# Kernel tuning notes

Measured on AMD Instinct MI355X. Metric: run time of the kernel, lower is better.

## Reference

```python
import jax, jax.numpy as jnp
import numpy as np
import math

B, H, L, D = 2, 16, 2048, 128


def setup_inputs() -> dict:
    key = jax.random.key(0)
    kq, kk, kv, km, kp = jax.random.split(key, 5)
    q = jax.random.normal(kq, (B, H, L, D), dtype=jnp.float32)
    k = jax.random.normal(kk, (B, H, L, D), dtype=jnp.float32)
    v = jax.random.normal(kv, (B, H, L, D), dtype=jnp.float32)
    mask = jax.random.randint(km, (B, 1, L, L), 0, 2, dtype=jnp.int32)
    probs = jax.random.uniform(kp, (B, L, L), dtype=jnp.float32)
    alpha = jnp.ones((), dtype=jnp.float32)  # learned scalar Parameter, init 1.0
    return {"q": q, "k": k, "v": v, "mask": mask, "probs": probs, "alpha": alpha}


def reference(q, k, v, mask, probs, alpha):
    # scores: (B, H, L, L)
    scale = 1.0 / math.sqrt(q.shape[-1])
    attn_score = jnp.einsum("bhqd,bhkd->bhqk", q, k) * scale
    # additive learned-scale probability bias, broadcast over heads
    attn_score = attn_score + probs[:, None, :, :] * alpha
    # masked_fill(mask == 0, -inf)
    attn_score = jnp.where(mask == 0, -jnp.inf, attn_score)
    attn_p = jax.nn.softmax(attn_score, axis=-1)
    # dropout p=0.0 -> identity
    attention = jnp.einsum("bhqk,bhkd->bhqd", attn_p, v)
    return attention, attn_p
```

## Files before the change

### kernel.cpp

```cpp
#include <hip/hip_runtime.h>

constexpr int BB = 2, HH = 16, LL = 2048, DD = 128;
constexpr int QB = 64, KB = 32, NKT = LL / KB;
constexpr float SCALE = 0.08838834764831845f;

typedef __attribute__((ext_vector_type(8))) short bf16x8;
typedef __attribute__((ext_vector_type(8))) unsigned short u16x8;
typedef __attribute__((ext_vector_type(4))) float f32x4;
typedef __attribute__((ext_vector_type(4))) int i32x4;

static __device__ __forceinline__ unsigned short f2bf(float f) {
  unsigned int u = __builtin_bit_cast(unsigned int, f);
  u += 0x7fffu + ((u >> 16) & 1u);
  return (unsigned short)(u >> 16);
}
static __device__ __forceinline__ float bf2f(unsigned short h) {
  return __builtin_bit_cast(float, (unsigned int)h << 16);
}

#define GLD16(gsrc, ldst) __builtin_amdgcn_global_load_lds( \
    (const __attribute__((address_space(1))) void*)(gsrc), \
    (__attribute__((address_space(3))) void*)(ldst), 16, 0, 0)

__global__ __launch_bounds__(256)
void prep_kernel(const float* __restrict__ k, const float* __restrict__ v,
                 const int* __restrict__ mask, const float* __restrict__ probs,
                 const float* __restrict__ alphap,
                 unsigned short* __restrict__ kbT, unsigned short* __restrict__ vtT,
                 unsigned short* __restrict__ biasW)
{
  __shared__ unsigned short sT[128 * 40];
  const int bid = blockIdx.x;
  const int bh = bid >> 6, kt = bid & 63;
  const int t = threadIdx.x;
  const float alpha = alphap[0];
  const size_t tileBase = (size_t)bid * 4096;
  const float* kg = k + ((size_t)bh * LL + kt * 32) * DD;
  const float* vg = v + ((size_t)bh * LL + kt * 32) * DD;

  #pragma unroll
  for (int s = t; s < 512; s += 256) {
    int dsl = s >> 5, key = s & 31;
    const float* src = kg + key * DD + dsl * 8;
    float4 a = *(const float4*)src;
    float4 c = *(const float4*)(src + 4);
    u16x8 w;
    w[0] = f2bf(a.x); w[1] = f2bf(a.y); w[2] = f2bf(a.z); w[3] = f2bf(a.w);
    w[4] = f2bf(c.x); w[5] = f2bf(c.y); w[6] = f2bf(c.z); w[7] = f2bf(c.w);
    *(u16x8*)(kbT + tileBase + (size_t)s * 8) = w;
  }
  #pragma unroll
  for (int i = 0; i < 4; ++i) {
    int idx = i * 256 + t;
    int key = idx >> 5, d4 = (idx & 31) * 4;
    float4 x = ((const float4*)vg)[idx];
    sT[(d4 + 0) * 40 + key] = f2bf(x.x);
    sT[(d4 + 1) * 40 + key] = f2bf(x.y);
    sT[(d4 + 2) * 40 + key] = f2bf(x.z);
    sT[(d4 + 3) * 40 + key] = f2bf(x.w);
  }
  #pragma unroll
  for (int it = 0; it < 2; ++it) {
    int tileIdx = bid * 2 + it;
    int b = tileIdx >> 11;
    int rem = tileIdx & 2047;
    int tq = rem >> 6;
    int tk = rem & 63;
    int row = ((t >> 6) << 4) + (t & 15);
    int kc = ((t >> 4) & 3) * 4;
    const float* pr = probs + (size_t)b * LL * LL + (size_t)(tq * 64 + row) * LL + tk * 32;
    const int* mr = mask + (size_t)b * LL * LL + (size_t)(tq * 64 + row) * LL + tk * 32;
    float4 f0 = *(const float4*)(pr + kc);
    float4 f1 = *(const float4*)(pr + kc + 16);
    int4 m0 = *(const int4*)(mr + kc);
    int4 m1 = *(const int4*)(mr + kc + 16);
    u16x8 o;
    o[0] = f2bf(m0.x ? f0.x * alpha : -1e30f);
    o[1] = f2bf(m0.y ? f0.y * alpha : -1e30f);
    o[2] = f2bf(m0.z ? f0.z * alpha : -1e30f);
    o[3] = f2bf(m0.w ? f0.w * alpha : -1e30f);
    o[4] = f2bf(m1.x ? f1.x * alpha : -1e30f);
    o[5] = f2bf(m1.y ? f1.y * alpha : -1e30f);
    o[6] = f2bf(m1.z ? f1.z * alpha : -1e30f);
    o[7] = f2bf(m1.w ? f1.w * alpha : -1e30f);
    *(u16x8*)(biasW + (size_t)tileIdx * 2048 + t * 8) = o;
  }
  __syncthreads();
  #pragma unroll
  for (int s = t; s < 512; s += 256) {
    int kc = s >> 7, d = s & 127;
    u16x8 w = *(const u16x8*)&sT[d * 40 + kc * 8];
    *(u16x8*)(vtT + tileBase + (size_t)s * 8) = w;
  }
}

__global__ __launch_bounds__(256, 6)
void passA_kernel(const float* __restrict__ q, const unsigned short* __restrict__ kbT,
                  const unsigned short* __restrict__ biasW, float* __restrict__ invW)
{
  __shared__ unsigned short sK[2][4096];

  const int tid = threadIdx.x;
  const int lane = tid & 63;
  const int wid = tid >> 6;
  const int l15 = lane & 15;
  const int l4 = lane >> 4;

  const int bid = blockIdx.x;
  const int work = ((bid & 7) << 7) | (bid >> 3);
  const int bh = work >> 5;
  const int qt = work & 31;
  const int b = bh >> 4;
  const int q0 = qt * QB;
  const int row16 = wid << 4;

  const unsigned short* kbh = kbT + (size_t)bh * 64 * 4096;
  const unsigned short* bg = biasW + ((size_t)(b * 32 + qt) * 64) * 2048 + (wid << 9) + (lane << 3);

  bf16x8 qf0, qf1, qf2, qf3;
  {
    const float* qs = q + (size_t)(bh * LL + q0 + row16 + l15) * DD + l4 * 8;
    #define LQ(FR, KC) { \
      float4 a = *(const float4*)(qs + (KC) * 32); \
      float4 c = *(const float4*)(qs + (KC) * 32 + 4); \
      FR[0]=(short)f2bf(a.x); FR[1]=(short)f2bf(a.y); FR[2]=(short)f2bf(a.z); FR[3]=(short)f2bf(a.w); \
      FR[4]=(short)f2bf(c.x); FR[5]=(short)f2bf(c.y); FR[6]=(short)f2bf(c.z); FR[7]=(short)f2bf(c.w); }
    LQ(qf0, 0) LQ(qf1, 1) LQ(qf2, 2) LQ(qf3, 3)
    #undef LQ
  }

  #define DMA_K(BUF, KT) do { \
    GLD16(kbh + (size_t)(KT) * 4096 + tid * 8,         &sK[BUF][wid << 9]); \
    GLD16(kbh + (size_t)(KT) * 4096 + (256 + tid) * 8, &sK[BUF][2048 + (wid << 9)]); } while (0)

  #define QKS(KC, QF) { \
    bf16x8 k0 = *(const bf16x8*)&sK[cur][(((KC) * 4 + l4) * 32 + l15) * 8]; \
    a0 = __builtin_amdgcn_mfma_f32_16x16x32_bf16(k0, QF, a0, 0, 0, 0); \
    bf16x8 k1 = *(const bf16x8*)&sK[cur][(((KC) * 4 + l4) * 32 + 16 + l15) * 8]; \
    a1 = __builtin_amdgcn_mfma_f32_16x16x32_bf16(k1, QF, a1, 0, 0, 0); }

  DMA_K(0, 0);
  u16x8 cnb = *(const u16x8*)(bg);
  float sum = 0.f;
  for (int kt = 0; kt < NKT; ++kt) {
    const int cur = kt & 1;
    __syncthreads();
    if (kt + 1 < NKT) DMA_K(cur ^ 1, kt + 1);
    u16x8 bt = cnb;
    if (kt + 1 < NKT) cnb = *(const u16x8*)(bg + (size_t)(kt + 1) * 2048);
    f32x4 a0 = {0.f,0.f,0.f,0.f}, a1 = {0.f,0.f,0.f,0.f};
    QKS(0, qf0) QKS(1, qf1) QKS(2, qf2) QKS(3, qf3)
    sum += __expf(a0[0] * SCALE + bf2f(bt[0]));
    sum += __expf(a0[1] * SCALE + bf2f(bt[1]));
    sum += __expf(a0[2] * SCALE + bf2f(bt[2]));
    sum += __expf(a0[3] * SCALE + bf2f(bt[3]));
    sum += __expf(a1[0] * SCALE + bf2f(bt[4]));
    sum += __expf(a1[1] * SCALE + bf2f(bt[5]));
    sum += __expf(a1[2] * SCALE + bf2f(bt[6]));
    sum += __expf(a1[3] * SCALE + bf2f(bt[7]));
  }
  sum += __shfl_xor(sum, 16, 64);
  sum += __shfl_xor(sum, 32, 64);
  if (l4 == 0)
    invW[(size_t)bh * LL + q0 + row16 + l15] = 1.0f / sum;
  #undef DMA_K
  #undef QKS
}

__global__ __launch_bounds__(256, 4)
void passB_kernel(const float* __restrict__ q, const unsigned short* __restrict__ kbT,
                  const unsigned short* __restrict__ vtT, const unsigned short* __restrict__ biasW,
                  const float* __restrict__ invW,
                  float* __restrict__ outA, float* __restrict__ outP)
{
  __shared__ unsigned short sK[2][4096];
  __shared__ unsigned short sVt[2][4096];

  const int tid = threadIdx.x;
  const int lane = tid & 63;
  const int wid = tid >> 6;
  const int l15 = lane & 15;
  const int l4 = lane >> 4;

  const int bid = blockIdx.x;
  const int work = ((bid & 7) << 7) | (bid >> 3);
  const int bh = work >> 5;
  const int qt = work & 31;
  const int b = bh >> 4;
  const int q0 = qt * QB;
  const int row16 = wid << 4;

  const unsigned short* kbh = kbT + (size_t)bh * 64 * 4096;
  const unsigned short* vbh = vtT + (size_t)bh * 64 * 4096;
  const unsigned short* bg = biasW + ((size_t)(b * 32 + qt) * 64) * 2048 + (wid << 9) + (lane << 3);
  float* oA = outA + (size_t)(bh * LL + q0) * DD;
  float* oPr = outP + (size_t)bh * LL * LL + (size_t)(q0 + row16 + l15) * LL;

  const float inv = invW[(size_t)bh * LL + q0 + row16 + l15];

  bf16x8 qf0, qf1, qf2, qf3;
  {
    const float* qs = q + (size_t)(bh * LL + q0 + row16 + l15) * DD + l4 * 8;
    #define LQ(FR, KC) { \
      float4 a = *(const float4*)(qs + (KC) * 32); \
      float4 c = *(const float4*)(qs + (KC) * 32 + 4); \
      FR[0]=(short)f2bf(a.x); FR[1]=(short)f2bf(a.y); FR[2]=(short)f2bf(a.z); FR[3]=(short)f2bf(a.w); \
      FR[4]=(short)f2bf(c.x); FR[5]=(short)f2bf(c.y); FR[6]=(short)f2bf(c.z); FR[7]=(short)f2bf(c.w); }
    LQ(qf0, 0) LQ(qf1, 1) LQ(qf2, 2) LQ(qf3, 3)
    #undef LQ
  }

  #define DMA_K(BUF, KT) do { \
    GLD16(kbh + (size_t)(KT) * 4096 + tid * 8,         &sK[BUF][wid << 9]); \
    GLD16(kbh + (size_t)(KT) * 4096 + (256 + tid) * 8, &sK[BUF][2048 + (wid << 9)]); } while (0)
  #define DMA_V(BUF, KT) do { \
    GLD16(vbh + (size_t)(KT) * 4096 + tid * 8,         &sVt[BUF][wid << 9]); \
    GLD16(vbh + (size_t)(KT) * 4096 + (256 + tid) * 8, &sVt[BUF][2048 + (wid << 9)]); } while (0)

  #define QKS(KC, QF) { \
    bf16x8 k0 = *(const bf16x8*)&sK[cur][(((KC) * 4 + l4) * 32 + l15) * 8]; \
    a0 = __builtin_amdgcn_mfma_f32_16x16x32_bf16(k0, QF, a0, 0, 0, 0); \
    bf16x8 k1 = *(const bf16x8*)&sK[cur][(((KC) * 4 + l4) * 32 + 16 + l15) * 8]; \
    a1 = __builtin_amdgcn_mfma_f32_16x16x32_bf16(k1, QF, a1, 0, 0, 0); }

  const int srcA = l15 + (((l4 << 1) + 0) & 3) * 16;
  const int srcB = l15 + (((l4 << 1) + 1) & 3) * 16;
  const bool hiTile = (l4 >= 2);

  f32x4 oacc[8];
  #pragma unroll
  for (int dt = 0; dt < 8; ++dt) oacc[dt] = (f32x4){0.f,0.f,0.f,0.f};

  u16x8 cnb;

  #define BBODY(KT) do { \
    const int cur = (KT) & 1; \
    u16x8 bt = cnb; \
    if ((KT) + 1 < NKT) cnb = *(const u16x8*)(bg + (size_t)((KT) + 1) * 2048); \
    f32x4 a0 = {0.f,0.f,0.f,0.f}, a1 = {0.f,0.f,0.f,0.f}; \
    QKS(0, qf0) QKS(1, qf1) QKS(2, qf2) QKS(3, qf3) \
    f32x4 p0, p1; \
    p0[0] = __expf(a0[0] * SCALE + bf2f(bt[0])) * inv; \
    p0[1] = __expf(a0[1] * SCALE + bf2f(bt[1])) * inv; \
    p0[2] = __expf(a0[2] * SCALE + bf2f(bt[2])) * inv; \
    p0[3] = __expf(a0[3] * SCALE + bf2f(bt[3])) * inv; \
    p1[0] = __expf(a1[0] * SCALE + bf2f(bt[4])) * inv; \
    p1[1] = __expf(a1[1] * SCALE + bf2f(bt[5])) * inv; \
    p1[2] = __expf(a1[2] * SCALE + bf2f(bt[6])) * inv; \
    p1[3] = __expf(a1[3] * SCALE + bf2f(bt[7])) * inv; \
    __builtin_nontemporal_store(p0, (f32x4*)(oPr + (KT) * 32 + (l4 << 2))); \
    __builtin_nontemporal_store(p1, (f32x4*)(oPr + (KT) * 32 + 16 + (l4 << 2))); \
    unsigned d00, d01, d10, d11; \
    asm("v_cvt_pk_bf16_f32 %0, %1, %2" : "=v"(d00) : "v"(p0[0]), "v"(p0[1])); \
    asm("v_cvt_pk_bf16_f32 %0, %1, %2" : "=v"(d01) : "v"(p0[2]), "v"(p0[3])); \
    asm("v_cvt_pk_bf16_f32 %0, %1, %2" : "=v"(d10) : "v"(p1[0]), "v"(p1[1])); \
    asm("v_cvt_pk_bf16_f32 %0, %1, %2" : "=v"(d11) : "v"(p1[2]), "v"(p1[3])); \
    int a00 = __shfl((int)d00, srcA, 64); \
    int a01 = __shfl((int)d01, srcA, 64); \
    int a02 = __shfl((int)d00, srcB, 64); \
    int a03 = __shfl((int)d01, srcB, 64); \
    int b00 = __shfl((int)d10, srcA, 64); \
    int b01 = __shfl((int)d11, srcA, 64); \
    int b02 = __shfl((int)d10, srcB, 64); \
    int b03 = __shfl((int)d11, srcB, 64); \
    i32x4 fw; \
    fw[0] = hiTile ? b00 : a00; \
    fw[1] = hiTile ? b01 : a01; \
    fw[2] = hiTile ? b02 : a02; \
    fw[3] = hiTile ? b03 : a03; \
    bf16x8 aP = __builtin_bit_cast(bf16x8, fw); \
    _Pragma("unroll") \
    for (int dt = 0; dt < 8; ++dt) { \
      bf16x8 bV = *(const bf16x8*)&sVt[cur][(l4 * 128 + dt * 16 + l15) * 8]; \
      oacc[dt] = __builtin_amdgcn_mfma_f32_16x16x32_bf16(aP, bV, oacc[dt], 0, 0, 0); \
    } \
  } while (0)

  cnb = *(const u16x8*)(bg);
  DMA_K(0, 0); DMA_V(0, 0);
  asm volatile("s_waitcnt vmcnt(0)\n\ts_barrier" ::: "memory");
  DMA_K(1, 1); DMA_V(1, 1);
  BBODY(0);
  for (int kt = 1; kt < NKT; ++kt) {
    asm volatile("s_waitcnt vmcnt(2)\n\ts_barrier" ::: "memory");
    if (kt + 1 < NKT) {
      const int c2 = (kt + 1) & 1;
      DMA_K(c2, kt + 1); DMA_V(c2, kt + 1);
    }
    BBODY(kt);
  }

  #pragma unroll
  for (int dt = 0; dt < 8; ++dt) {
    #pragma unroll
    for (int r = 0; r < 4; ++r) {
      __builtin_nontemporal_store(oacc[dt][r],
          oA + (size_t)(row16 + (l4 << 2) + r) * DD + dt * 16 + l15);
    }
  }
}

extern "C" void kernel_launch(void* const* d_in, const int* in_sizes, int n_in,
                              void* d_out, int out_size, void* d_ws, size_t ws_size,
                              hipStream_t stream) {
  const float* q = (const float*)d_in[0];
  const float* k = (const float*)d_in[1];
  const float* v = (const float*)d_in[2];
  const int* mask = (const int*)d_in[3];
  const float* probs = (const float*)d_in[4];
  const float* alpha = (const float*)d_in[5];
  float* outA = (float*)d_out;
  float* outP = outA + (size_t)BB * HH * LL * DD;
  unsigned short* kbT = (unsigned short*)d_ws;
  unsigned short* vtT = kbT + (size_t)32 * 64 * 4096;
  unsigned short* biasW = vtT + (size_t)32 * 64 * 4096;
  float* invW = (float*)(biasW + (size_t)4096 * 2048);
  hipLaunchKernelGGL(prep_kernel, dim3(32 * 64), dim3(256), 0, stream,
                     k, v, mask, probs, alpha, kbT, vtT, biasW);
  hipLaunchKernelGGL(passA_kernel, dim3(BB * HH * (LL / QB)), dim3(256), 0, stream,
                     q, kbT, biasW, invW);
  hipLaunchKernelGGL(passB_kernel, dim3(BB * HH * (LL / QB)), dim3(256), 0, stream,
                     q, kbT, vtT, biasW, invW, outA, outP);
}
```

Before: 257.8 us.

## Switch attention passes to 32x32x16 MFMA with two-wave blocks

Replaces the 16x16x32 bf16 MFMA tiles in both softmax passes with 32x32x16 MFMA, so each wave now owns 32 query rows and blocks shrink to 128 threads. The bias workspace layout in the prep kernel is permuted to match the new accumulator layout, and the P-to-A-operand reshuffle becomes a single xor-32 swap. The aim is to cut LDS K/V fragment reads and shuffle overhead per flop. In exchange each thread holds more accumulator registers, and the probability stores become narrower strided writes.

```diff
diff --git a/kernel.cpp b/kernel.cpp
--- a/kernel.cpp
+++ b/kernel.cpp
@@ -7,6 +7,7 @@
 typedef __attribute__((ext_vector_type(8))) short bf16x8;
 typedef __attribute__((ext_vector_type(8))) unsigned short u16x8;
 typedef __attribute__((ext_vector_type(4))) float f32x4;
+typedef __attribute__((ext_vector_type(16))) float f32x16;
 typedef __attribute__((ext_vector_type(4))) int i32x4;
 
 static __device__ __forceinline__ unsigned short f2bf(float f) {
@@ -61,19 +62,22 @@
   }
   #pragma unroll
   for (int it = 0; it < 2; ++it) {
-    int tileIdx = bid * 2 + it;
-    int b = tileIdx >> 11;
-    int rem = tileIdx & 2047;
-    int tq = rem >> 6;
-    int tk = rem & 63;
-    int row = ((t >> 6) << 4) + (t & 15);
-    int kc = ((t >> 4) & 3) * 4;
-    const float* pr = probs + (size_t)b * LL * LL + (size_t)(tq * 64 + row) * LL + tk * 32;
-    const int* mr = mask + (size_t)b * LL * LL + (size_t)(tq * 64 + row) * LL + tk * 32;
-    float4 f0 = *(const float4*)(pr + kc);
-    float4 f1 = *(const float4*)(pr + kc + 16);
-    int4 m0 = *(const int4*)(mr + kc);
-    int4 m1 = *(const int4*)(mr + kc + 16);
+    int ti = bid * 2 + it;
+    int b = ti >> 11;
+    int tq = (ti >> 6) & 31;
+    int tk = ti & 63;
+    int wv = t >> 7;
+    int ln = (t >> 1) & 63;
+    int rh = t & 1;
+    int l31 = ln & 31, hi = ln >> 5;
+    int qrow = tq * 64 + wv * 32 + l31;
+    int kbase = tk * 32 + 4 * hi + rh * 16;
+    const float* pr = probs + (size_t)b * LL * LL + (size_t)qrow * LL + kbase;
+    const int* mr = mask + (size_t)b * LL * LL + (size_t)qrow * LL + kbase;
+    float4 f0 = *(const float4*)(pr);
+    float4 f1 = *(const float4*)(pr + 8);
+    int4 m0 = *(const int4*)(mr);
+    int4 m1 = *(const int4*)(mr + 8);
     u16x8 o;
     o[0] = f2bf(m0.x ? f0.x * alpha : -1e30f);
     o[1] = f2bf(m0.y ? f0.y * alpha : -1e30f);
@@ -83,7 +87,7 @@
     o[5] = f2bf(m1.y ? f1.y * alpha : -1e30f);
     o[6] = f2bf(m1.z ? f1.z * alpha : -1e30f);
     o[7] = f2bf(m1.w ? f1.w * alpha : -1e30f);
-    *(u16x8*)(biasW + (size_t)tileIdx * 2048 + t * 8) = o;
+    *(u16x8*)(biasW + (size_t)ti * 2048 + wv * 1024 + ln * 16 + rh * 8) = o;
   }
   __syncthreads();
   #pragma unroll
@@ -94,80 +98,104 @@
   }
 }
 
-__global__ __launch_bounds__(256, 6)
+#define ZERO16 {0.f,0.f,0.f,0.f,0.f,0.f,0.f,0.f,0.f,0.f,0.f,0.f,0.f,0.f,0.f,0.f}
+
+#define COMMON_DECODE \
+  const int tid = threadIdx.x; \
+  const int lane = tid & 63; \
+  const int wid = tid >> 6; \
+  const int l31 = lane & 31; \
+  const int hi5 = lane >> 5; \
+  const int bid = blockIdx.x; \
+  const int work = ((bid & 7) << 7) | (bid >> 3); \
+  const int bh = work >> 5; \
+  const int qt = work & 31; \
+  const int b = bh >> 4; \
+  const int q0 = qt * QB; \
+  const int qrow = q0 + wid * 32 + l31;
+
+#define LOAD_QFRAGS \
+  bf16x8 qf0, qf1, qf2, qf3, qf4, qf5, qf6, qf7; \
+  { \
+    const float* qs = q + (size_t)(bh * LL + qrow) * DD + hi5 * 8; \
+    _Pragma("unroll") \
+    for (int m = 0; m < 8; ++m) { \
+      float4 a = *(const float4*)(qs + m * 16); \
+      float4 c = *(const float4*)(qs + m * 16 + 4); \
+      u16x8 w; \
+      w[0]=f2bf(a.x); w[1]=f2bf(a.y); w[2]=f2bf(a.z); w[3]=f2bf(a.w); \
+      w[4]=f2bf(c.x); w[5]=f2bf(c.y); w[6]=f2bf(c.z); w[7]=f2bf(c.w); \
+      bf16x8 f = __builtin_bit_cast(bf16x8, w); \
+      switch (m) { case 0: qf0=f; break; case 1: qf1=f; break; \
+                   case 2: qf2=f; break; case 3: qf3=f; break; \
+                   case 4: qf4=f; break; case 5: qf5=f; break; \
+                   case 6: qf6=f; break; default: qf7=f; } \
+    } \
+  }
+
+#define DMA_T(ARR, BASE, KT) do { \
+  _Pragma("unroll") \
+  for (int i_ = 0; i_ < 4; ++i_) \
+    GLD16((BASE) + (size_t)(KT) * 4096 + (i_ * 128 + tid) * 8, \
+          &ARR[i_ * 1024 + (tid >> 6) * 512]); } while (0)
+
+#define QK32(SBUF) \
+  f32x16 s = ZERO16; \
+  { \
+    bf16x8 kf; \
+    kf = *(const bf16x8*)&SBUF[(( 0 + hi5) * 32 + l31) * 8]; \
+    s = __builtin_amdgcn_mfma_f32_32x32x16_bf16(kf, qf0, s, 0, 0, 0); \
+    kf = *(const bf16x8*)&SBUF[(( 2 + hi5) * 32 + l31) * 8]; \
+    s = __builtin_amdgcn_mfma_f32_32x32x16_bf16(kf, qf1, s, 0, 0, 0); \
+    kf = *(const bf16x8*)&SBUF[(( 4 + hi5) * 32 + l31) * 8]; \
+    s = __builtin_amdgcn_mfma_f32_32x32x16_bf16(kf, qf2, s, 0, 0, 0); \
+    kf = *(const bf16x8*)&SBUF[(( 6 + hi5) * 32 + l31) * 8]; \
+    s = __builtin_amdgcn_mfma_f32_32x32x16_bf16(kf, qf3, s, 0, 0, 0); \
+    kf = *(const bf16x8*)&SBUF[(( 8 + hi5) * 32 + l31) * 8]; \
+    s = __builtin_amdgcn_mfma_f32_32x32x16_bf16(kf, qf4, s, 0, 0, 0); \
+    kf = *(const bf16x8*)&SBUF[((10 + hi5) * 32 + l31) * 8]; \
+    s = __builtin_amdgcn_mfma_f32_32x32x16_bf16(kf, qf5, s, 0, 0, 0); \
+    kf = *(const bf16x8*)&SBUF[((12 + hi5) * 32 + l31) * 8]; \
+    s = __builtin_amdgcn_mfma_f32_32x32x16_bf16(kf, qf6, s, 0, 0, 0); \
+    kf = *(const bf16x8*)&SBUF[((14 + hi5) * 32 + l31) * 8]; \
+    s = __builtin_amdgcn_mfma_f32_32x32x16_bf16(kf, qf7, s, 0, 0, 0); \
+  }
+
+__global__ __launch_bounds__(128, 4)
 void passA_kernel(const float* __restrict__ q, const unsigned short* __restrict__ kbT,
                   const unsigned short* __restrict__ biasW, float* __restrict__ invW)
 {
   __shared__ unsigned short sK[2][4096];
-
-  const int tid = threadIdx.x;
-  const int lane = tid & 63;
-  const int wid = tid >> 6;
-  const int l15 = lane & 15;
-  const int l4 = lane >> 4;
-
-  const int bid = blockIdx.x;
-  const int work = ((bid & 7) << 7) | (bid >> 3);
-  const int bh = work >> 5;
-  const int qt = work & 31;
-  const int b = bh >> 4;
-  const int q0 = qt * QB;
-  const int row16 = wid << 4;
-
+  COMMON_DECODE
   const unsigned short* kbh = kbT + (size_t)bh * 64 * 4096;
-  const unsigned short* bg = biasW + ((size_t)(b * 32 + qt) * 64) * 2048 + (wid << 9) + (lane << 3);
-
-  bf16x8 qf0, qf1, qf2, qf3;
-  {
-    const float* qs = q + (size_t)(bh * LL + q0 + row16 + l15) * DD + l4 * 8;
-    #define LQ(FR, KC) { \
-      float4 a = *(const float4*)(qs + (KC) * 32); \
-      float4 c = *(const float4*)(qs + (KC) * 32 + 4); \
-      FR[0]=(short)f2bf(a.x); FR[1]=(short)f2bf(a.y); FR[2]=(short)f2bf(a.z); FR[3]=(short)f2bf(a.w); \
-      FR[4]=(short)f2bf(c.x); FR[5]=(short)f2bf(c.y); FR[6]=(short)f2bf(c.z); FR[7]=(short)f2bf(c.w); }
-    LQ(qf0, 0) LQ(qf1, 1) LQ(qf2, 2) LQ(qf3, 3)
-    #undef LQ
-  }
-
-  #define DMA_K(BUF, KT) do { \
-    GLD16(kbh + (size_t)(KT) * 4096 + tid * 8,         &sK[BUF][wid << 9]); \
-    GLD16(kbh + (size_t)(KT) * 4096 + (256 + tid) * 8, &sK[BUF][2048 + (wid << 9)]); } while (0)
-
-  #define QKS(KC, QF) { \
-    bf16x8 k0 = *(const bf16x8*)&sK[cur][(((KC) * 4 + l4) * 32 + l15) * 8]; \
-    a0 = __builtin_amdgcn_mfma_f32_16x16x32_bf16(k0, QF, a0, 0, 0, 0); \
-    bf16x8 k1 = *(const bf16x8*)&sK[cur][(((KC) * 4 + l4) * 32 + 16 + l15) * 8]; \
-    a1 = __builtin_amdgcn_mfma_f32_16x16x32_bf16(k1, QF, a1, 0, 0, 0); }
-
-  DMA_K(0, 0);
-  u16x8 cnb = *(const u16x8*)(bg);
+  const unsigned short* bg = biasW + ((size_t)(b * 32 + qt) * 64) * 2048 + wid * 1024 + lane * 16;
+  LOAD_QFRAGS
+
+  DMA_T(sK[0], kbh, 0);
+  u16x8 cb0 = *(const u16x8*)(bg);
+  u16x8 cb1 = *(const u16x8*)(bg + 8);
   float sum = 0.f;
   for (int kt = 0; kt < NKT; ++kt) {
     const int cur = kt & 1;
     __syncthreads();
-    if (kt + 1 < NKT) DMA_K(cur ^ 1, kt + 1);
-    u16x8 bt = cnb;
-    if (kt + 1 < NKT) cnb = *(const u16x8*)(bg + (size_t)(kt + 1) * 2048);
-    f32x4 a0 = {0.f,0.f,0.f,0.f}, a1 = {0.f,0.f,0.f,0.f};
-    QKS(0, qf0) QKS(1, qf1) QKS(2, qf2) QKS(3, qf3)
-    sum += __expf(a0[0] * SCALE + bf2f(bt[0]));
-    sum += __expf(a0[1] * SCALE + bf2f(bt[1]));
-    sum += __expf(a0[2] * SCALE + bf2f(bt[2]));
-    sum += __expf(a0[3] * SCALE + bf2f(bt[3]));
-    sum += __expf(a1[0] * SCALE + bf2f(bt[4]));
-    sum += __expf(a1[1] * SCALE + bf2f(bt[5]));
-    sum += __expf(a1[2] * SCALE + bf2f(bt[6]));
-    sum += __expf(a1[3] * SCALE + bf2f(bt[7]));
-  }
-  sum += __shfl_xor(sum, 16, 64);
+    if (kt + 1 < NKT) DMA_T(sK[cur ^ 1], kbh, kt + 1);
+    u16x8 b0 = cb0, b1 = cb1;
+    if (kt + 1 < NKT) {
+      cb0 = *(const u16x8*)(bg + (size_t)(kt + 1) * 2048);
+      cb1 = *(const u16x8*)(bg + (size_t)(kt + 1) * 2048 + 8);
+    }
+    QK32(sK[cur])
+    #pragma unroll
+    for (int r = 0; r < 8; ++r) sum += __expf(s[r] * SCALE + bf2f(b0[r]));
+    #pragma unroll
+    for (int r = 0; r < 8; ++r) sum += __expf(s[r + 8] * SCALE + bf2f(b1[r]));
+  }
   sum += __shfl_xor(sum, 32, 64);
-  if (l4 == 0)
-    invW[(size_t)bh * LL + q0 + row16 + l15] = 1.0f / sum;
-  #undef DMA_K
-  #undef QKS
-}
-
-__global__ __launch_bounds__(256, 4)
+  if (lane < 32)
+    invW[(size_t)bh * LL + qrow] = 1.0f / sum;
+}
+
+__global__ __launch_bounds__(128, 3)
 void passB_kernel(const float* __restrict__ q, const unsigned short* __restrict__ kbT,
                   const unsigned short* __restrict__ vtT, const unsigned short* __restrict__ biasW,
                   const float* __restrict__ invW,
@@ -175,129 +203,109 @@
 {
   __shared__ unsigned short sK[2][4096];
   __shared__ unsigned short sVt[2][4096];
-
-  const int tid = threadIdx.x;
-  const int lane = tid & 63;
-  const int wid = tid >> 6;
-  const int l15 = lane & 15;
-  const int l4 = lane >> 4;
-
-  const int bid = blockIdx.x;
-  const int work = ((bid & 7) << 7) | (bid >> 3);
-  const int bh = work >> 5;
-  const int qt = work & 31;
-  const int b = bh >> 4;
-  const int q0 = qt * QB;
-  const int row16 = wid << 4;
-
+  COMMON_DECODE
   const unsigned short* kbh = kbT + (size_t)bh * 64 * 4096;
   const unsigned short* vbh = vtT + (size_t)bh * 64 * 4096;
-  const unsigned short* bg = biasW + ((size_t)(b * 32 + qt) * 64) * 2048 + (wid << 9) + (lane << 3);
+  const unsigned short* bg = biasW + ((size_t)(b * 32 + qt) * 64) * 2048 + wid * 1024 + lane * 16;
   float* oA = outA + (size_t)(bh * LL + q0) * DD;
-  float* oPr = outP + (size_t)bh * LL * LL + (size_t)(q0 + row16 + l15) * LL;
-
-  const float inv = invW[(size_t)bh * LL + q0 + row16 + l15];
-
-  bf16x8 qf0, qf1, qf2, qf3;
-  {
-    const float* qs = q + (size_t)(bh * LL + q0 + row16 + l15) * DD + l4 * 8;
-    #define LQ(FR, KC) { \
-      float4 a = *(const float4*)(qs + (KC) * 32); \
-      float4 c = *(const float4*)(qs + (KC) * 32 + 4); \
-      FR[0]=(short)f2bf(a.x); FR[1]=(short)f2bf(a.y); FR[2]=(short)f2bf(a.z); FR[3]=(short)f2bf(a.w); \
-      FR[4]=(short)f2bf(c.x); FR[5]=(short)f2bf(c.y); FR[6]=(short)f2bf(c.z); FR[7]=(short)f2bf(c.w); }
-    LQ(qf0, 0) LQ(qf1, 1) LQ(qf2, 2) LQ(qf3, 3)
-    #undef LQ
-  }
-
-  #define DMA_K(BUF, KT) do { \
-    GLD16(kbh + (size_t)(KT) * 4096 + tid * 8,         &sK[BUF][wid << 9]); \
-    GLD16(kbh + (size_t)(KT) * 4096 + (256 + tid) * 8, &sK[BUF][2048 + (wid << 9)]); } while (0)
-  #define DMA_V(BUF, KT) do { \
-    GLD16(vbh + (size_t)(KT) * 4096 + tid * 8,         &sVt[BUF][wid << 9]); \
-    GLD16(vbh + (size_t)(KT) * 4096 + (256 + tid) * 8, &sVt[BUF][2048 + (wid << 9)]); } while (0)
-
-  #define QKS(KC, QF) { \
-    bf16x8 k0 = *(const bf16x8*)&sK[cur][(((KC) * 4 + l4) * 32 + l15) * 8]; \
-    a0 = __builtin_amdgcn_mfma_f32_16x16x32_bf16(k0, QF, a0, 0, 0, 0); \
-    bf16x8 k1 = *(const bf16x8*)&sK[cur][(((KC) * 4 + l4) * 32 + 16 + l15) * 8]; \
-    a1 = __builtin_amdgcn_mfma_f32_16x16x32_bf16(k1, QF, a1, 0, 0, 0); }
-
-  const int srcA = l15 + (((l4 << 1) + 0) & 3) * 16;
-  const int srcB = l15 + (((l4 << 1) + 1) & 3) * 16;
-  const bool hiTile = (l4 >= 2);
-
-  f32x4 oacc[8];
-  #pragma unroll
-  for (int dt = 0; dt < 8; ++dt) oacc[dt] = (f32x4){0.f,0.f,0.f,0.f};
-
-  u16x8 cnb;
+  float* oPr = outP + (size_t)bh * LL * LL + (size_t)qrow * LL;
+  const float inv = invW[(size_t)bh * LL + qrow];
+  LOAD_QFRAGS
+
+  f32x16 acc0 = ZERO16, acc1 = ZERO16, acc2 = ZERO16, acc3 = ZERO16;
+  u16x8 cb0, cb1;
 
   #define BBODY(KT) do { \
     const int cur = (KT) & 1; \
-    u16x8 bt = cnb; \
-    if ((KT) + 1 < NKT) cnb = *(const u16x8*)(bg + (size_t)((KT) + 1) * 2048); \
-    f32x4 a0 = {0.f,0.f,0.f,0.f}, a1 = {0.f,0.f,0.f,0.f}; \
-    QKS(0, qf0) QKS(1, qf1) QKS(2, qf2) QKS(3, qf3) \
-    f32x4 p0, p1; \
-    p0[0] = __expf(a0[0] * SCALE + bf2f(bt[0])) * inv; \
-    p0[1] = __expf(a0[1] * SCALE + bf2f(bt[1])) * inv; \
-    p0[2] = __expf(a0[2] * SCALE + bf2f(bt[2])) * inv; \
-    p0[3] = __expf(a0[3] * SCALE + bf2f(bt[3])) * inv; \
-    p1[0] = __expf(a1[0] * SCALE + bf2f(bt[4])) * inv; \
-    p1[1] = __expf(a1[1] * SCALE + bf2f(bt[5])) * inv; \
-    p1[2] = __expf(a1[2] * SCALE + bf2f(bt[6])) * inv; \
-    p1[3] = __expf(a1[3] * SCALE + bf2f(bt[7])) * inv; \
-    __builtin_nontemporal_store(p0, (f32x4*)(oPr + (KT) * 32 + (l4 << 2))); \
-    __builtin_nontemporal_store(p1, (f32x4*)(oPr + (KT) * 32 + 16 + (l4 << 2))); \
-    unsigned d00, d01, d10, d11; \
-    asm("v_cvt_pk_bf16_f32 %0, %1, %2" : "=v"(d00) : "v"(p0[0]), "v"(p0[1])); \
-    asm("v_cvt_pk_bf16_f32 %0, %1, %2" : "=v"(d01) : "v"(p0[2]), "v"(p0[3])); \
-    asm("v_cvt_pk_bf16_f32 %0, %1, %2" : "=v"(d10) : "v"(p1[0]), "v"(p1[1])); \
-    asm("v_cvt_pk_bf16_f32 %0, %1, %2" : "=v"(d11) : "v"(p1[2]), "v"(p1[3])); \
-    int a00 = __shfl((int)d00, srcA, 64); \
-    int a01 = __shfl((int)d01, srcA, 64); \
-    int a02 = __shfl((int)d00, srcB, 64); \
-    int a03 = __shfl((int)d01, srcB, 64); \
-    int b00 = __shfl((int)d10, srcA, 64); \
-    int b01 = __shfl((int)d11, srcA, 64); \
-    int b02 = __shfl((int)d10, srcB, 64); \
-    int b03 = __shfl((int)d11, srcB, 64); \
-    i32x4 fw; \
-    fw[0] = hiTile ? b00 : a00; \
-    fw[1] = hiTile ? b01 : a01; \
-    fw[2] = hiTile ? b02 : a02; \
-    fw[3] = hiTile ? b03 : a03; \
-    bf16x8 aP = __builtin_bit_cast(bf16x8, fw); \
+    u16x8 b0 = cb0, b1 = cb1; \
+    if ((KT) + 1 < NKT) { \
+      cb0 = *(const u16x8*)(bg + (size_t)((KT) + 1) * 2048); \
+      cb1 = *(const u16x8*)(bg + (size_t)((KT) + 1) * 2048 + 8); \
+    } \
+    QK32(sK[cur]) \
+    f32x16 p; \
     _Pragma("unroll") \
-    for (int dt = 0; dt < 8; ++dt) { \
-      bf16x8 bV = *(const bf16x8*)&sVt[cur][(l4 * 128 + dt * 16 + l15) * 8]; \
-      oacc[dt] = __builtin_amdgcn_mfma_f32_16x16x32_bf16(aP, bV, oacc[dt], 0, 0, 0); \
+    for (int r = 0; r < 8; ++r) p[r] = __expf(s[r] * SCALE + bf2f(b0[r])) * inv; \
+    _Pragma("unroll") \
+    for (int r = 0; r < 8; ++r) p[r + 8] = __expf(s[r + 8] * SCALE + bf2f(b1[r])) * inv; \
+     \
+    { \
+      f32x4 st; \
+      st[0]=p[0];  st[1]=p[1];  st[2]=p[2];  st[3]=p[3]; \
+      __builtin_nontemporal_store(st, (f32x4*)(oPr + (KT) * 32 + 4 * hi5)); \
+      st[0]=p[4];  st[1]=p[5];  st[2]=p[6];  st[3]=p[7]; \
+      __builtin_nontemporal_store(st, (f32x4*)(oPr + (KT) * 32 + 8 + 4 * hi5)); \
+      st[0]=p[8];  st[1]=p[9];  st[2]=p[10]; st[3]=p[11]; \
+      __builtin_nontemporal_store(st, (f32x4*)(oPr + (KT) * 32 + 16 + 4 * hi5)); \
+      st[0]=p[12]; st[1]=p[13]; st[2]=p[14]; st[3]=p[15]; \
+      __builtin_nontemporal_store(st, (f32x4*)(oPr + (KT) * 32 + 24 + 4 * hi5)); \
     } \
+     \
+    unsigned D0,D1,D2,D3,D4,D5,D6,D7; \
+    asm("v_cvt_pk_bf16_f32 %0, %1, %2" : "=v"(D0) : "v"(p[0]),  "v"(p[1])); \
+    asm("v_cvt_pk_bf16_f32 %0, %1, %2" : "=v"(D1) : "v"(p[2]),  "v"(p[3])); \
+    asm("v_cvt_pk_bf16_f32 %0, %1, %2" : "=v"(D2) : "v"(p[4]),  "v"(p[5])); \
+    asm("v_cvt_pk_bf16_f32 %0, %1, %2" : "=v"(D3) : "v"(p[6]),  "v"(p[7])); \
+    asm("v_cvt_pk_bf16_f32 %0, %1, %2" : "=v"(D4) : "v"(p[8]),  "v"(p[9])); \
+    asm("v_cvt_pk_bf16_f32 %0, %1, %2" : "=v"(D5) : "v"(p[10]), "v"(p[11])); \
+    asm("v_cvt_pk_bf16_f32 %0, %1, %2" : "=v"(D6) : "v"(p[12]), "v"(p[13])); \
+    asm("v_cvt_pk_bf16_f32 %0, %1, %2" : "=v"(D7) : "v"(p[14]), "v"(p[15])); \
+    int X0 = __shfl_xor((int)D0, 32, 64), X1 = __shfl_xor((int)D1, 32, 64); \
+    int X2 = __shfl_xor((int)D2, 32, 64), X3 = __shfl_xor((int)D3, 32, 64); \
+    int X4 = __shfl_xor((int)D4, 32, 64), X5 = __shfl_xor((int)D5, 32, 64); \
+    int X6 = __shfl_xor((int)D6, 32, 64), X7 = __shfl_xor((int)D7, 32, 64); \
+    const bool lo = (hi5 == 0); \
+    i32x4 w0, w1; \
+    w0[0] = lo ? (int)D0 : X2;  w0[1] = lo ? (int)D1 : X3; \
+    w0[2] = lo ? X0 : (int)D2;  w0[3] = lo ? X1 : (int)D3; \
+    w1[0] = lo ? (int)D4 : X6;  w1[1] = lo ? (int)D5 : X7; \
+    w1[2] = lo ? X4 : (int)D6;  w1[3] = lo ? X5 : (int)D7; \
+    bf16x8 aP0 = __builtin_bit_cast(bf16x8, w0); \
+    bf16x8 aP1 = __builtin_bit_cast(bf16x8, w1); \
+     \
+    bf16x8 bV; \
+    bV = *(const bf16x8*)&sVt[cur][((0 + hi5) * 128 +  0 + l31) * 8]; \
+    acc0 = __builtin_amdgcn_mfma_f32_32x32x16_bf16(aP0, bV, acc0, 0, 0, 0); \
+    bV = *(const bf16x8*)&sVt[cur][((2 + hi5) * 128 +  0 + l31) * 8]; \
+    acc0 = __builtin_amdgcn_mfma_f32_32x32x16_bf16(aP1, bV, acc0, 0, 0, 0); \
+    bV = *(const bf16x8*)&sVt[cur][((0 + hi5) * 128 + 32 + l31) * 8]; \
+    acc1 = __builtin_amdgcn_mfma_f32_32x32x16_bf16(aP0, bV, acc1, 0, 0, 0); \
+    bV = *(const bf16x8*)&sVt[cur][((2 + hi5) * 128 + 32 + l31) * 8]; \
+    acc1 = __builtin_amdgcn_mfma_f32_32x32x16_bf16(aP1, bV, acc1, 0, 0, 0); \
+    bV = *(const bf16x8*)&sVt[cur][((0 + hi5) * 128 + 64 + l31) * 8]; \
+    acc2 = __builtin_amdgcn_mfma_f32_32x32x16_bf16(aP0, bV, acc2, 0, 0, 0); \
+    bV = *(const bf16x8*)&sVt[cur][((2 + hi5) * 128 + 64 + l31) * 8]; \
+    acc2 = __builtin_amdgcn_mfma_f32_32x32x16_bf16(aP1, bV, acc2, 0, 0, 0); \
+    bV = *(const bf16x8*)&sVt[cur][((0 + hi5) * 128 + 96 + l31) * 8]; \
+    acc3 = __builtin_amdgcn_mfma_f32_32x32x16_bf16(aP0, bV, acc3, 0, 0, 0); \
+    bV = *(const bf16x8*)&sVt[cur][((2 + hi5) * 128 + 96 + l31) * 8]; \
+    acc3 = __builtin_amdgcn_mfma_f32_32x32x16_bf16(aP1, bV, acc3, 0, 0, 0); \
   } while (0)
 
-  cnb = *(const u16x8*)(bg);
-  DMA_K(0, 0); DMA_V(0, 0);
+  cb0 = *(const u16x8*)(bg);
+  cb1 = *(const u16x8*)(bg + 8);
+  DMA_T(sK[0], kbh, 0); DMA_T(sVt[0], vbh, 0);
   asm volatile("s_waitcnt vmcnt(0)\n\ts_barrier" ::: "memory");
-  DMA_K(1, 1); DMA_V(1, 1);
+  DMA_T(sK[1], kbh, 1); DMA_T(sVt[1], vbh, 1);
   BBODY(0);
   for (int kt = 1; kt < NKT; ++kt) {
-    asm volatile("s_waitcnt vmcnt(2)\n\ts_barrier" ::: "memory");
+    asm volatile("s_waitcnt vmcnt(4)\n\ts_barrier" ::: "memory");
     if (kt + 1 < NKT) {
       const int c2 = (kt + 1) & 1;
-      DMA_K(c2, kt + 1); DMA_V(c2, kt + 1);
+      DMA_T(sK[c2], kbh, kt + 1); DMA_T(sVt[c2], vbh, kt + 1);
     }
     BBODY(kt);
   }
 
-  #pragma unroll
-  for (int dt = 0; dt < 8; ++dt) {
-    #pragma unroll
-    for (int r = 0; r < 4; ++r) {
-      __builtin_nontemporal_store(oacc[dt][r],
-          oA + (size_t)(row16 + (l4 << 2) + r) * DD + dt * 16 + l15);
+  #define STA(ACC, DC) \
+    _Pragma("unroll") \
+    for (int r = 0; r < 16; ++r) { \
+      int qr = (r & 3) + 8 * (r >> 2) + 4 * hi5; \
+      __builtin_nontemporal_store(ACC[r], \
+          oA + (size_t)(wid * 32 + qr) * DD + (DC) * 32 + l31); \
     }
-  }
+  STA(acc0, 0) STA(acc1, 1) STA(acc2, 2) STA(acc3, 3)
+  #undef STA
 }
 
 extern "C" void kernel_launch(void* const* d_in, const int* in_sizes, int n_in,
@@ -317,8 +325,8 @@
   float* invW = (float*)(biasW + (size_t)4096 * 2048);
   hipLaunchKernelGGL(prep_kernel, dim3(32 * 64), dim3(256), 0, stream,
                      k, v, mask, probs, alpha, kbT, vtT, biasW);
-  hipLaunchKernelGGL(passA_kernel, dim3(BB * HH * (LL / QB)), dim3(256), 0, stream,
+  hipLaunchKernelGGL(passA_kernel, dim3(BB * HH * (LL / QB)), dim3(128), 0, stream,
                      q, kbT, biasW, invW);
-  hipLaunchKernelGGL(passB_kernel, dim3(BB * HH * (LL / QB)), dim3(256), 0, stream,
+  hipLaunchKernelGGL(passB_kernel, dim3(BB * HH * (LL / QB)), dim3(128), 0, stream,
                      q, kbT, vtT, biasW, invW, outA, outP);
 }
```

After: 474.8 us. 84.2% more time.
